# Kernel optimization log

Measured on AMD Instinct MI355X. Metric: run time of the kernel, lower is better.

The kernel has to match this reference:

```python
import jax, jax.numpy as jnp
import numpy as np

IN_DIM = 1024
OUT_DIM = 1024


def setup_inputs() -> dict:
    key = jax.random.key(0)
    k1, k2, k3, k4 = jax.random.split(key, 4)
    B, T = 4, 2048
    x = jax.random.normal(k1, (B, T, IN_DIM), dtype=jnp.float32)
    # torch Linear stores weight as [out, in]; y = x @ W.T
    s = 1.0 / np.sqrt(IN_DIM)
    Wq = jax.random.uniform(k2, (OUT_DIM, IN_DIM), jnp.float32, -s, s)
    Wk = jax.random.uniform(k3, (OUT_DIM, IN_DIM), jnp.float32, -s, s)
    Wv = jax.random.uniform(k4, (OUT_DIM, IN_DIM), jnp.float32, -s, s)
    return {"x": x, "Wq": Wq, "Wk": Wk, "Wv": Wv}


def reference(x, Wq, Wk, Wv):
    # x: [B, T, D_in]
    q = jnp.einsum('btd,od->bto', x, Wq)   # [B, T, D_out]
    k = jnp.einsum('btd,od->bto', x, Wk)
    v = jnp.einsum('btd,od->bto', x, Wv)
    T = x.shape[1]
    scores = jnp.einsum('bqo,bko->bqk', q, k)  # [B, T, T]
    causal = jnp.tril(jnp.ones((T, T), dtype=bool))  # True = keep
    scores = jnp.where(causal, scores, -jnp.inf)
    scale = 1.0 / jnp.sqrt(jnp.asarray(k.shape[-1], scores.dtype))
    weights = jax.nn.softmax(scores * scale, axis=-1)
    # dropout_value = 0.0 -> identity
    return jnp.einsum('bqk,bko->bqo', weights, v)
```

## Files before the change

kernel.cpp:

```cpp
#include <hip/hip_runtime.h>
#include <cstdint>
#include <cstddef>
#include <cmath>

typedef __attribute__((ext_vector_type(8))) short bf16x8;
typedef __attribute__((ext_vector_type(4))) float f32x4;

#define CSCALE 0.045084220027780106f

__device__ __forceinline__ void gload_lds16(const void* g, void* l) {
  __builtin_amdgcn_global_load_lds(
      (const __attribute__((address_space(1))) unsigned int*)g,
      (__attribute__((address_space(3))) unsigned int*)l, 16, 0, 0);
}

__device__ __forceinline__ unsigned short f2bf(float f) {
  unsigned int u = __float_as_uint(f);
  return (unsigned short)((u + 0x7FFFu + ((u >> 16) & 1u)) >> 16);
}

__device__ __forceinline__ float bf2f(unsigned short u) {
  return __uint_as_float((unsigned int)u << 16);
}

__global__ void cvt_kernel(const float* __restrict__ in,
                           unsigned short* __restrict__ out, int n8) {
  int i = blockIdx.x * blockDim.x + threadIdx.x;
  if (i >= n8) return;
  const float4* p = (const float4*)in + (size_t)i * 2;
  float4 a = p[0], b = p[1];
  float vals[8] = {a.x, a.y, a.z, a.w, b.x, b.y, b.z, b.w};
  union { unsigned short u[8]; uint4 v; } r;
#pragma unroll
  for (int j = 0; j < 8; ++j) r.u[j] = f2bf(vals[j]);
  ((uint4*)out)[i] = r.v;
}

__global__ void cvt3_kernel(const float* __restrict__ a,
                            const float* __restrict__ b,
                            const float* __restrict__ c,
                            unsigned short* __restrict__ oa,
                            unsigned short* __restrict__ ob,
                            unsigned short* __restrict__ oc) {
  int bid = blockIdx.x;
  const float* src;
  unsigned short* dst;
  int base;
  if (bid < 512) { src = a; dst = oa; base = bid; }
  else if (bid < 1024) { src = b; dst = ob; base = bid - 512; }
  else { src = c; dst = oc; base = bid - 1024; }
  int i = base * 256 + threadIdx.x;
  const float4* p = (const float4*)src + (size_t)i * 2;
  float4 x = p[0], y = p[1];
  float vals[8] = {x.x, x.y, x.z, x.w, y.x, y.y, y.z, y.w};
  union { unsigned short u[8]; uint4 v; } r;
#pragma unroll
  for (int j = 0; j < 8; ++j) r.u[j] = f2bf(vals[j]);
  ((uint4*)dst)[i] = r.v;
}

template <int MODE>
__device__ __forceinline__ void gemm_body(const unsigned short* __restrict__ A,
                                          const unsigned short* __restrict__ B,
                                          void* __restrict__ Cv) {
  constexpr int LDA = (MODE <= 1) ? 1024 : 2048;
  constexpr int LDB = (MODE <= 1) ? 1024 : (MODE == 2 ? 2048 : 8192);
  constexpr int LDC =
      (MODE == 0) ? 2048 : (MODE == 1 ? 8192 : (MODE == 2 ? 2048 : 1024));
  constexpr int NWG = (MODE == 0) ? 512 : (MODE == 2 ? 288 : 256);

  const int wg = ((int)blockIdx.x & 7) * (NWG >> 3) + ((int)blockIdx.x >> 3);

  int arow, brow, NT = 16, kb = 0;
  size_t cbase;
  if constexpr (MODE == 0) {
    int bm = wg & 31, bn = wg >> 5;
    arow = bm * 256; brow = bn * 128;
    cbase = (size_t)arow * LDC + bn * 128;
  } else if constexpr (MODE == 1) {
    int bm = wg & 3, bn = wg >> 2;
    arow = bm * 256; brow = bn * 128;
    cbase = (size_t)arow * LDC + bn * 128;
  } else if constexpr (MODE == 2) {
    int b = wg / 72, e = wg % 72;
    int qt = (int)((sqrtf(4.f * (float)e + 1.f) - 1.f) * 0.5f);
    if ((qt + 1) * (qt + 2) <= e) ++qt;
    if (qt * (qt + 1) > e) --qt;
    int jt = e - qt * (qt + 1);
    arow = b * 2048 + qt * 256;
    brow = b * 2048 + jt * 128;
    cbase = (size_t)arow * LDC + jt * 128;
  } else {
    int n = wg & 7, r = wg >> 3;
    int b = r >> 3, qt = 7 - (r & 7);
    arow = b * 2048 + qt * 256;
    brow = n * 128;
    kb = b * 2048;
    NT = (qt + 1) * 4;
    cbase = (size_t)arow * LDC + n * 128;
  }

  __shared__ char lds[3][49152];
  const int tid = threadIdx.x, lane = tid & 63;
  const int l15 = lane & 15, g = lane >> 4;
  const int w = tid >> 6, wm = w >> 2, wn = w & 3;

  f32x4 acc[8][2] = {};

  auto stageA1 = [&](int slot, int t2, int i) {
    int chunk = i * 512 + tid;
    int row = chunk >> 3;
    int c8 = (chunk & 7) ^ (row & 7);
    gload_lds16(A + (size_t)(arow + row) * LDA + t2 * 64 + c8 * 8,
                &lds[slot][(chunk & ~63) * 16]);
  };
  auto stageB1 = [&](int slot, int t2, int i) {
    int chunk = i * 512 + tid;
    int row = chunk >> 3;
    int c8 = (chunk & 7) ^ (row & 7);
    gload_lds16(B + (size_t)(brow + row) * LDB + kb + t2 * 64 + c8 * 8,
                &lds[slot][32768 + (chunk & ~63) * 16]);
  };
  auto lda_frag = [&](int slot, int mt, int kk) -> bf16x8 {
    int row = wm * 128 + mt * 16 + l15;
    int byte = row * 128 + ((kk * 64 + g * 16) ^ ((l15 & 7) << 4));
    return *(const bf16x8*)&lds[slot][byte];
  };
  auto ldb_frag = [&](int slot, int n2, int kk) -> bf16x8 {
    int row = wn * 32 + n2 * 16 + l15;
    int byte = 32768 + row * 128 + ((kk * 64 + g * 16) ^ ((l15 & 7) << 4));
    return *(const bf16x8*)&lds[slot][byte];
  };

#pragma unroll
  for (int i = 0; i < 4; ++i) stageA1(0, 0, i);
#pragma unroll
  for (int i = 0; i < 2; ++i) stageB1(0, 0, i);
#pragma unroll
  for (int i = 0; i < 4; ++i) stageA1(1, 1, i);
#pragma unroll
  for (int i = 0; i < 2; ++i) stageB1(1, 1, i);
  asm volatile("s_waitcnt vmcnt(6)" ::: "memory");
  __builtin_amdgcn_s_barrier();

  int slot = 0;
  for (int j = 0; j < NT; ++j) {
    const int ss = (slot >= 1) ? slot - 1 : 2;
    const bool st = (j + 2) < NT;
    bf16x8 bv[2][2], af[4][2];
#pragma unroll
    for (int n2 = 0; n2 < 2; ++n2)
#pragma unroll
      for (int kk = 0; kk < 2; ++kk) bv[n2][kk] = ldb_frag(slot, n2, kk);
#pragma unroll
    for (int mt = 0; mt < 4; ++mt)
#pragma unroll
      for (int kk = 0; kk < 2; ++kk) af[mt][kk] = lda_frag(slot, mt, kk);
    if (st) { stageA1(ss, j + 2, 0); stageA1(ss, j + 2, 1); stageA1(ss, j + 2, 2); }
    __builtin_amdgcn_s_barrier();
    asm volatile("s_waitcnt lgkmcnt(0)" ::: "memory");
    __builtin_amdgcn_sched_barrier(0);
    __builtin_amdgcn_s_setprio(1);
#pragma unroll
    for (int mt = 0; mt < 4; ++mt)
#pragma unroll
      for (int n2 = 0; n2 < 2; ++n2)
#pragma unroll
        for (int kk = 0; kk < 2; ++kk)
          acc[mt][n2] = __builtin_amdgcn_mfma_f32_16x16x32_bf16(
              af[mt][kk], bv[n2][kk], acc[mt][n2], 0, 0, 0);
    __builtin_amdgcn_s_setprio(0);
    __builtin_amdgcn_s_barrier();
#pragma unroll
    for (int mt = 0; mt < 4; ++mt)
#pragma unroll
      for (int kk = 0; kk < 2; ++kk) af[mt][kk] = lda_frag(slot, 4 + mt, kk);
    if (st) { stageA1(ss, j + 2, 3); stageB1(ss, j + 2, 0); stageB1(ss, j + 2, 1); }
    __builtin_amdgcn_s_barrier();
    asm volatile("s_waitcnt lgkmcnt(0)" ::: "memory");
    __builtin_amdgcn_sched_barrier(0);
    __builtin_amdgcn_s_setprio(1);
#pragma unroll
    for (int mt = 0; mt < 4; ++mt)
#pragma unroll
      for (int n2 = 0; n2 < 2; ++n2)
#pragma unroll
        for (int kk = 0; kk < 2; ++kk)
          acc[4 + mt][n2] = __builtin_amdgcn_mfma_f32_16x16x32_bf16(
              af[mt][kk], bv[n2][kk], acc[4 + mt][n2], 0, 0, 0);
    __builtin_amdgcn_s_setprio(0);
    if (st) {
      asm volatile("s_waitcnt vmcnt(6)" ::: "memory");
    } else if (j + 2 == NT) {
      asm volatile("s_waitcnt vmcnt(0)" ::: "memory");
    }
    __builtin_amdgcn_s_barrier();
    slot = (slot == 2) ? 0 : slot + 1;
  }

#pragma unroll
  for (int mt = 0; mt < 8; ++mt) {
#pragma unroll
    for (int r = 0; r < 4; ++r) {
      int ro = wm * 128 + mt * 16 + g * 4 + r;
      int co = wn * 32 + l15;
      if constexpr (MODE == 3) {
        float* Cp = (float*)Cv + cbase + (size_t)ro * LDC + co;
        Cp[0] = acc[mt][0][r];
        Cp[16] = acc[mt][1][r];
      } else {
        unsigned short* Cp = (unsigned short*)Cv + cbase + (size_t)ro * LDC + co;
        Cp[0] = f2bf(acc[mt][0][r]);
        Cp[16] = f2bf(acc[mt][1][r]);
      }
    }
  }
}

__global__ __launch_bounds__(512, 2) void gemm_proj(
    const unsigned short* __restrict__ A, const unsigned short* __restrict__ B,
    void* __restrict__ C) { gemm_body<0>(A, B, C); }
__global__ __launch_bounds__(512, 2) void gemm_vt(
    const unsigned short* __restrict__ A, const unsigned short* __restrict__ B,
    void* __restrict__ C) { gemm_body<1>(A, B, C); }
__global__ __launch_bounds__(512, 2) void gemm_s(
    const unsigned short* __restrict__ A, const unsigned short* __restrict__ B,
    void* __restrict__ C) { gemm_body<2>(A, B, C); }
__global__ __launch_bounds__(512, 2) void gemm_pv(
    const unsigned short* __restrict__ A, const unsigned short* __restrict__ B,
    void* __restrict__ C) { gemm_body<3>(A, B, C); }

__global__ __launch_bounds__(256) void softmax_kernel(
    unsigned short* __restrict__ S) {
  const int r = blockIdx.x * 4 + (threadIdx.x >> 6);
  const int lane = threadIdx.x & 63;
  const int q = r & 2047;
  unsigned short* row = S + (size_t)r * 2048;
  const int klen = q + 1;
  const int kmax = ((q >> 8) + 1) << 8;

  float v[4][8];
  float m = -__builtin_inff();
#pragma unroll
  for (int it = 0; it < 4; ++it) {
    int base = (lane + it * 64) * 8;
    if (base < klen) {
      bf16x8 u = *(const bf16x8*)(row + base);
#pragma unroll
      for (int e = 0; e < 8; ++e) {
        float f = bf2f((unsigned short)u[e]) * CSCALE;
        v[it][e] = (base + e <= q) ? f : -__builtin_inff();
        m = fmaxf(m, v[it][e]);
      }
    } else {
#pragma unroll
      for (int e = 0; e < 8; ++e) v[it][e] = -__builtin_inff();
    }
  }
#pragma unroll
  for (int s = 1; s < 64; s <<= 1) m = fmaxf(m, __shfl_xor(m, s));

  float lsum = 0.f;
#pragma unroll
  for (int it = 0; it < 4; ++it)
#pragma unroll
    for (int e = 0; e < 8; ++e) {
      float p = exp2f(v[it][e] - m);
      v[it][e] = p;
      lsum += p;
    }
#pragma unroll
  for (int s = 1; s < 64; s <<= 1) lsum += __shfl_xor(lsum, s);
  float inv = 1.0f / lsum;

#pragma unroll
  for (int it = 0; it < 4; ++it) {
    int base = (lane + it * 64) * 8;
    if (base < kmax) {
      union { unsigned short u[8]; uint4 x; } o;
#pragma unroll
      for (int e = 0; e < 8; ++e) o.u[e] = f2bf(v[it][e] * inv);
      *(uint4*)(row + base) = o.x;
    }
  }
}

extern "C" void kernel_launch(void* const* d_in, const int* in_sizes, int n_in,
                              void* d_out, int out_size, void* d_ws,
                              size_t ws_size, hipStream_t stream) {
  const float* x = (const float*)d_in[0];
  const float* Wq = (const float*)d_in[1];
  const float* Wk = (const float*)d_in[2];
  const float* Wv = (const float*)d_in[3];
  unsigned short* ws = (unsigned short*)d_ws;
  unsigned short* xb = ws;
  unsigned short* Wqk = ws + (size_t)(8u << 20);
  unsigned short* Wvb = ws + (size_t)(10u << 20);
  unsigned short* QKb = ws + (size_t)(11u << 20);
  unsigned short* Vtb = ws + (size_t)(27u << 20);
  unsigned short* Sb = ws + (size_t)(35u << 20);

  cvt_kernel<<<4096, 256, 0, stream>>>(x, xb, 1048576);
  cvt3_kernel<<<1536, 256, 0, stream>>>(Wq, Wk, Wv, Wqk,
                                        Wqk + (size_t)(1u << 20), Wvb);
  gemm_proj<<<512, 512, 0, stream>>>(xb, Wqk, QKb);
  gemm_vt<<<256, 512, 0, stream>>>(Wvb, xb, Vtb);
  gemm_s<<<288, 512, 0, stream>>>(QKb, QKb + 1024, Sb);
  softmax_kernel<<<2048, 256, 0, stream>>>(Sb);
  gemm_pv<<<256, 512, 0, stream>>>(Sb, Vtb, (float*)d_out);
}
```

Baseline: 249.1 us.

## Use 256x256 GEMM tiles with double buffering and split-K for causal PV

Enlarges the GEMM output tile from 256x128 to 256x256 and switches from triple to double buffered LDS staging. The fetch schedule is reworked into three phases per k-step. It drops the XCD-aware block remapping and halves the grid sizes. For the causal PV GEMM, the longer query tiles are split along K into two halves: one half writes partials to the workspace and a new fixup kernel adds them into the output. The aim is more data reuse per tile and better load balance, at the cost of a smaller grid (under one wave on 256 CUs), more accumulator registers, an extra kernel launch and extra partial-sum traffic.

```diff
diff --git a/kernel.cpp b/kernel.cpp
--- a/kernel.cpp
+++ b/kernel.cpp
@@ -62,140 +62,162 @@
 template <int MODE>
 __device__ __forceinline__ void gemm_body(const unsigned short* __restrict__ A,
                                           const unsigned short* __restrict__ B,
-                                          void* __restrict__ Cv) {
+                                          void* __restrict__ Cv,
+                                          float* __restrict__ Cpart) {
   constexpr int LDA = (MODE <= 1) ? 1024 : 2048;
   constexpr int LDB = (MODE <= 1) ? 1024 : (MODE == 2 ? 2048 : 8192);
   constexpr int LDC =
       (MODE == 0) ? 2048 : (MODE == 1 ? 8192 : (MODE == 2 ? 2048 : 1024));
-  constexpr int NWG = (MODE == 0) ? 512 : (MODE == 2 ? 288 : 256);
-
-  const int wg = ((int)blockIdx.x & 7) * (NWG >> 3) + ((int)blockIdx.x >> 3);
-
-  int arow, brow, NT = 16, kb = 0;
+
+  int arow, brow, NT = 16, kA = 0, kB = 0;
   size_t cbase;
+  bool toPart = false;
   if constexpr (MODE == 0) {
-    int bm = wg & 31, bn = wg >> 5;
-    arow = bm * 256; brow = bn * 128;
-    cbase = (size_t)arow * LDC + bn * 128;
+    int bm = blockIdx.x & 31, bn = blockIdx.x >> 5;
+    arow = bm * 256; brow = bn * 256;
+    cbase = (size_t)arow * LDC + bn * 256;
   } else if constexpr (MODE == 1) {
-    int bm = wg & 3, bn = wg >> 2;
-    arow = bm * 256; brow = bn * 128;
-    cbase = (size_t)arow * LDC + bn * 128;
+    int bm = blockIdx.x & 3, bn = blockIdx.x >> 2;
+    arow = bm * 256; brow = bn * 256;
+    cbase = (size_t)arow * LDC + bn * 256;
   } else if constexpr (MODE == 2) {
-    int b = wg / 72, e = wg % 72;
-    int qt = (int)((sqrtf(4.f * (float)e + 1.f) - 1.f) * 0.5f);
-    if ((qt + 1) * (qt + 2) <= e) ++qt;
-    if (qt * (qt + 1) > e) --qt;
-    int jt = e - qt * (qt + 1);
+    int b = blockIdx.x / 36, e = blockIdx.x % 36;
+    int qt = (int)((sqrtf(8.f * (float)e + 1.f) - 1.f) * 0.5f);
+    if ((qt + 1) * (qt + 2) / 2 <= e) ++qt;
+    if (qt * (qt + 1) / 2 > e) --qt;
+    int jt = e - qt * (qt + 1) / 2;
     arow = b * 2048 + qt * 256;
-    brow = b * 2048 + jt * 128;
-    cbase = (size_t)arow * LDC + jt * 128;
+    brow = b * 2048 + jt * 256;
+    cbase = (size_t)arow * LDC + jt * 256;
   } else {
-    int n = wg & 7, r = wg >> 3;
-    int b = r >> 3, qt = 7 - (r & 7);
+    int bn = blockIdx.x & 3, u = blockIdx.x >> 2;
+    int b = u / 12, ub = u % 12;
+    int qt, half;
+    if (ub < 4) { qt = ub; half = -1; NT = (qt + 1) * 4; kA = 0; }
+    else { int idx = ub - 4; qt = 4 + (idx >> 1); half = idx & 1;
+           NT = (qt + 1) * 2; kA = half * NT * 64; }
     arow = b * 2048 + qt * 256;
-    brow = n * 128;
-    kb = b * 2048;
-    NT = (qt + 1) * 4;
-    cbase = (size_t)arow * LDC + n * 128;
-  }
-
-  __shared__ char lds[3][49152];
+    brow = bn * 256;
+    kB = b * 2048 + kA;
+    toPart = (half == 1);
+    cbase = toPart ? ((size_t)(b * 1024 + (qt - 4) * 256) * 1024 + bn * 256)
+                   : ((size_t)arow * 1024 + bn * 256);
+  }
+
+  __shared__ char lds[2][65536];
   const int tid = threadIdx.x, lane = tid & 63;
   const int l15 = lane & 15, g = lane >> 4;
   const int w = tid >> 6, wm = w >> 2, wn = w & 3;
 
-  f32x4 acc[8][2] = {};
-
-  auto stageA1 = [&](int slot, int t2, int i) {
+  f32x4 acc[8][4] = {};
+
+  auto stageA = [&](int d, int t, int i) {
     int chunk = i * 512 + tid;
     int row = chunk >> 3;
     int c8 = (chunk & 7) ^ (row & 7);
-    gload_lds16(A + (size_t)(arow + row) * LDA + t2 * 64 + c8 * 8,
-                &lds[slot][(chunk & ~63) * 16]);
+    gload_lds16(A + (size_t)(arow + row) * LDA + kA + t * 64 + c8 * 8,
+                &lds[d][(chunk & ~63) * 16]);
   };
-  auto stageB1 = [&](int slot, int t2, int i) {
+  auto stageB = [&](int d, int t, int i) {
     int chunk = i * 512 + tid;
     int row = chunk >> 3;
     int c8 = (chunk & 7) ^ (row & 7);
-    gload_lds16(B + (size_t)(brow + row) * LDB + kb + t2 * 64 + c8 * 8,
-                &lds[slot][32768 + (chunk & ~63) * 16]);
+    gload_lds16(B + (size_t)(brow + row) * LDB + kB + t * 64 + c8 * 8,
+                &lds[d][32768 + (chunk & ~63) * 16]);
   };
-  auto lda_frag = [&](int slot, int mt, int kk) -> bf16x8 {
+  auto lda_frag = [&](int d, int mt, int kk) -> bf16x8 {
     int row = wm * 128 + mt * 16 + l15;
-    int byte = row * 128 + ((kk * 64 + g * 16) ^ ((l15 & 7) << 4));
-    return *(const bf16x8*)&lds[slot][byte];
+    int byte = row * 128 + (((kk * 4 + g) ^ (l15 & 7)) << 4);
+    return *(const bf16x8*)&lds[d][byte];
   };
-  auto ldb_frag = [&](int slot, int n2, int kk) -> bf16x8 {
-    int row = wn * 32 + n2 * 16 + l15;
-    int byte = 32768 + row * 128 + ((kk * 64 + g * 16) ^ ((l15 & 7) << 4));
-    return *(const bf16x8*)&lds[slot][byte];
+  auto ldb_frag = [&](int d, int nf, int kk) -> bf16x8 {
+    int row = wn * 64 + nf * 16 + l15;
+    int byte = 32768 + row * 128 + (((kk * 4 + g) ^ (l15 & 7)) << 4);
+    return *(const bf16x8*)&lds[d][byte];
   };
 
 #pragma unroll
-  for (int i = 0; i < 4; ++i) stageA1(0, 0, i);
-#pragma unroll
-  for (int i = 0; i < 2; ++i) stageB1(0, 0, i);
-#pragma unroll
-  for (int i = 0; i < 4; ++i) stageA1(1, 1, i);
-#pragma unroll
-  for (int i = 0; i < 2; ++i) stageB1(1, 1, i);
-  asm volatile("s_waitcnt vmcnt(6)" ::: "memory");
+  for (int i = 0; i < 4; ++i) stageA(0, 0, i);
+#pragma unroll
+  for (int i = 0; i < 4; ++i) stageB(0, 0, i);
+#pragma unroll
+  for (int i = 0; i < 4; ++i) stageA(1, 1, i);
+#pragma unroll
+  for (int i = 0; i < 4; ++i) stageB(1, 1, i);
+  asm volatile("s_waitcnt vmcnt(8)" ::: "memory");
   __builtin_amdgcn_s_barrier();
 
-  int slot = 0;
   for (int j = 0; j < NT; ++j) {
-    const int ss = (slot >= 1) ? slot - 1 : 2;
+    const int d = j & 1;
     const bool st = (j + 2) < NT;
-    bf16x8 bv[2][2], af[4][2];
-#pragma unroll
-    for (int n2 = 0; n2 < 2; ++n2)
-#pragma unroll
-      for (int kk = 0; kk < 2; ++kk) bv[n2][kk] = ldb_frag(slot, n2, kk);
-#pragma unroll
-    for (int mt = 0; mt < 4; ++mt)
-#pragma unroll
-      for (int kk = 0; kk < 2; ++kk) af[mt][kk] = lda_frag(slot, mt, kk);
-    if (st) { stageA1(ss, j + 2, 0); stageA1(ss, j + 2, 1); stageA1(ss, j + 2, 2); }
-    __builtin_amdgcn_s_barrier();
+    bf16x8 af0[4][2], af1[4][2], bv[4][2];
+#pragma unroll
+    for (int mt = 0; mt < 4; ++mt)
+#pragma unroll
+      for (int kk = 0; kk < 2; ++kk) af0[mt][kk] = lda_frag(d, mt, kk);
+#pragma unroll
+    for (int nf = 0; nf < 2; ++nf)
+#pragma unroll
+      for (int kk = 0; kk < 2; ++kk) bv[nf][kk] = ldb_frag(d, nf, kk);
     asm volatile("s_waitcnt lgkmcnt(0)" ::: "memory");
     __builtin_amdgcn_sched_barrier(0);
+    __builtin_amdgcn_s_barrier();
+    if (st) { stageA(d, j + 2, 0); stageA(d, j + 2, 2); }
+#pragma unroll
+    for (int nf = 2; nf < 4; ++nf)
+#pragma unroll
+      for (int kk = 0; kk < 2; ++kk) bv[nf][kk] = ldb_frag(d, nf, kk);
     __builtin_amdgcn_s_setprio(1);
 #pragma unroll
     for (int mt = 0; mt < 4; ++mt)
 #pragma unroll
-      for (int n2 = 0; n2 < 2; ++n2)
+      for (int nf = 0; nf < 2; ++nf)
 #pragma unroll
         for (int kk = 0; kk < 2; ++kk)
-          acc[mt][n2] = __builtin_amdgcn_mfma_f32_16x16x32_bf16(
-              af[mt][kk], bv[n2][kk], acc[mt][n2], 0, 0, 0);
+          acc[mt][nf] = __builtin_amdgcn_mfma_f32_16x16x32_bf16(
+              af0[mt][kk], bv[nf][kk], acc[mt][nf], 0, 0, 0);
     __builtin_amdgcn_s_setprio(0);
-    __builtin_amdgcn_s_barrier();
-#pragma unroll
-    for (int mt = 0; mt < 4; ++mt)
-#pragma unroll
-      for (int kk = 0; kk < 2; ++kk) af[mt][kk] = lda_frag(slot, 4 + mt, kk);
-    if (st) { stageA1(ss, j + 2, 3); stageB1(ss, j + 2, 0); stageB1(ss, j + 2, 1); }
-    __builtin_amdgcn_s_barrier();
     asm volatile("s_waitcnt lgkmcnt(0)" ::: "memory");
     __builtin_amdgcn_sched_barrier(0);
+    __builtin_amdgcn_s_barrier();
+    if (st) {
+      stageB(d, j + 2, 0); stageB(d, j + 2, 1);
+      stageB(d, j + 2, 2); stageB(d, j + 2, 3);
+    }
+#pragma unroll
+    for (int mt = 0; mt < 4; ++mt)
+#pragma unroll
+      for (int kk = 0; kk < 2; ++kk) af1[mt][kk] = lda_frag(d, 4 + mt, kk);
     __builtin_amdgcn_s_setprio(1);
 #pragma unroll
     for (int mt = 0; mt < 4; ++mt)
 #pragma unroll
-      for (int n2 = 0; n2 < 2; ++n2)
+      for (int nf = 2; nf < 4; ++nf)
 #pragma unroll
         for (int kk = 0; kk < 2; ++kk)
-          acc[4 + mt][n2] = __builtin_amdgcn_mfma_f32_16x16x32_bf16(
-              af[mt][kk], bv[n2][kk], acc[4 + mt][n2], 0, 0, 0);
+          acc[mt][nf] = __builtin_amdgcn_mfma_f32_16x16x32_bf16(
+              af0[mt][kk], bv[nf][kk], acc[mt][nf], 0, 0, 0);
+    __builtin_amdgcn_s_setprio(0);
+    asm volatile("s_waitcnt lgkmcnt(0)" ::: "memory");
+    __builtin_amdgcn_sched_barrier(0);
+    __builtin_amdgcn_s_barrier();
+    if (st) { stageA(d, j + 2, 1); stageA(d, j + 2, 3); }
+    __builtin_amdgcn_s_setprio(1);
+#pragma unroll
+    for (int mt = 0; mt < 4; ++mt)
+#pragma unroll
+      for (int nf = 0; nf < 4; ++nf)
+#pragma unroll
+        for (int kk = 0; kk < 2; ++kk)
+          acc[4 + mt][nf] = __builtin_amdgcn_mfma_f32_16x16x32_bf16(
+              af1[mt][kk], bv[nf][kk], acc[4 + mt][nf], 0, 0, 0);
     __builtin_amdgcn_s_setprio(0);
     if (st) {
-      asm volatile("s_waitcnt vmcnt(6)" ::: "memory");
+      asm volatile("s_waitcnt vmcnt(8)" ::: "memory");
     } else if (j + 2 == NT) {
       asm volatile("s_waitcnt vmcnt(0)" ::: "memory");
     }
     __builtin_amdgcn_s_barrier();
-    slot = (slot == 2) ? 0 : slot + 1;
   }
 
 #pragma unroll
@@ -203,15 +225,17 @@
 #pragma unroll
     for (int r = 0; r < 4; ++r) {
       int ro = wm * 128 + mt * 16 + g * 4 + r;
-      int co = wn * 32 + l15;
+      int co = wn * 64 + l15;
       if constexpr (MODE == 3) {
-        float* Cp = (float*)Cv + cbase + (size_t)ro * LDC + co;
-        Cp[0] = acc[mt][0][r];
-        Cp[16] = acc[mt][1][r];
+        float* base = toPart ? Cpart : (float*)Cv;
+        float* Cp = base + cbase + (size_t)ro * LDC + co;
+#pragma unroll
+        for (int nf = 0; nf < 4; ++nf) Cp[nf * 16] = acc[mt][nf][r];
       } else {
-        unsigned short* Cp = (unsigned short*)Cv + cbase + (size_t)ro * LDC + co;
-        Cp[0] = f2bf(acc[mt][0][r]);
-        Cp[16] = f2bf(acc[mt][1][r]);
+        unsigned short* Cp =
+            (unsigned short*)Cv + cbase + (size_t)ro * LDC + co;
+#pragma unroll
+        for (int nf = 0; nf < 4; ++nf) Cp[nf * 16] = f2bf(acc[mt][nf][r]);
       }
     }
   }
@@ -219,16 +243,30 @@
 
 __global__ __launch_bounds__(512, 2) void gemm_proj(
     const unsigned short* __restrict__ A, const unsigned short* __restrict__ B,
-    void* __restrict__ C) { gemm_body<0>(A, B, C); }
+    void* __restrict__ C) { gemm_body<0>(A, B, C, nullptr); }
 __global__ __launch_bounds__(512, 2) void gemm_vt(
     const unsigned short* __restrict__ A, const unsigned short* __restrict__ B,
-    void* __restrict__ C) { gemm_body<1>(A, B, C); }
+    void* __restrict__ C) { gemm_body<1>(A, B, C, nullptr); }
 __global__ __launch_bounds__(512, 2) void gemm_s(
     const unsigned short* __restrict__ A, const unsigned short* __restrict__ B,
-    void* __restrict__ C) { gemm_body<2>(A, B, C); }
+    void* __restrict__ C) { gemm_body<2>(A, B, C, nullptr); }
 __global__ __launch_bounds__(512, 2) void gemm_pv(
     const unsigned short* __restrict__ A, const unsigned short* __restrict__ B,
-    void* __restrict__ C) { gemm_body<3>(A, B, C); }
+    void* __restrict__ C, float* __restrict__ Cpart) {
+  gemm_body<3>(A, B, C, Cpart);
+}
+
+__global__ __launch_bounds__(256) void fixup_kernel(
+    float* __restrict__ Out, const float* __restrict__ Part) {
+  int j = blockIdx.x * 256 + threadIdx.x;
+  int row = j >> 8, c4 = j & 255;
+  int b = row >> 10, r = row & 1023;
+  float4* o = (float4*)(Out + (size_t)(b * 2048 + 1024 + r) * 1024) + c4;
+  const float4* p = (const float4*)(Part + (size_t)row * 1024) + c4;
+  float4 a = *o, q = *p;
+  a.x += q.x; a.y += q.y; a.z += q.z; a.w += q.w;
+  *o = a;
+}
 
 __global__ __launch_bounds__(256) void softmax_kernel(
     unsigned short* __restrict__ S) {
@@ -299,13 +337,15 @@
   unsigned short* QKb = ws + (size_t)(11u << 20);
   unsigned short* Vtb = ws + (size_t)(27u << 20);
   unsigned short* Sb = ws + (size_t)(35u << 20);
+  float* Ppart = (float*)d_ws;
 
   cvt_kernel<<<4096, 256, 0, stream>>>(x, xb, 1048576);
   cvt3_kernel<<<1536, 256, 0, stream>>>(Wq, Wk, Wv, Wqk,
                                         Wqk + (size_t)(1u << 20), Wvb);
-  gemm_proj<<<512, 512, 0, stream>>>(xb, Wqk, QKb);
-  gemm_vt<<<256, 512, 0, stream>>>(Wvb, xb, Vtb);
-  gemm_s<<<288, 512, 0, stream>>>(QKb, QKb + 1024, Sb);
+  gemm_proj<<<256, 512, 0, stream>>>(xb, Wqk, QKb);
+  gemm_vt<<<128, 512, 0, stream>>>(Wvb, xb, Vtb);
+  gemm_s<<<144, 512, 0, stream>>>(QKb, QKb + 1024, Sb);
   softmax_kernel<<<2048, 256, 0, stream>>>(Sb);
-  gemm_pv<<<256, 512, 0, stream>>>(Sb, Vtb, (float*)d_out);
-}
+  gemm_pv<<<192, 512, 0, stream>>>(Sb, Vtb, (float*)d_out, Ppart);
+  fixup_kernel<<<4096, 256, 0, stream>>>((float*)d_out, Ppart);
+}
```

Result: no change. 246.2 us (-1.2%).
